# Kernel tuning notes

Measured on AMD Instinct MI355X. Metric: run time of the kernel, lower is better.

The kernel has to match this reference:

```python
import jax, jax.numpy as jnp
import numpy as np
from jax import lax

N, H, C_IN, G, E_CLS, N_ACT = 8192, 128, 3, 40, 16, 5
FLAT = 8 * 8 * 32  # conv output 8x8x32 for grid_size=40


def _conv(x, w, b, stride):
    y = lax.conv_general_dilated(x, w, (stride, stride), 'VALID',
                                 dimension_numbers=('NCHW', 'OIHW', 'NCHW'))
    return y + b[None, :, None, None]


def setup_inputs() -> dict:
    key = jax.random.key(0)
    ks = jax.random.split(key, 24)
    s = 0.05
    return {
        'img_batch': jax.random.normal(ks[0], (N, C_IN, G, G), jnp.float32),
        'adjacency': jax.random.randint(ks[1], (N, N), 0, 2, jnp.int32),
        'class_ids': jax.random.randint(ks[2], (N,), 0, 2, jnp.int64),
        'hidden_state': jax.random.normal(ks[3], (N, H), jnp.float32),
        'conv1_w': jax.random.normal(ks[4], (16, C_IN, 5, 5), jnp.float32) * s,
        'conv1_b': jnp.zeros((16,), jnp.float32),
        'conv2_w': jax.random.normal(ks[5], (32, 16, 3, 3), jnp.float32) * s,
        'conv2_b': jnp.zeros((32,), jnp.float32),
        'fc_vis_w': jax.random.normal(ks[6], (H, FLAT), jnp.float32) * s,
        'fc_vis_b': jnp.zeros((H,), jnp.float32),
        'embed_table': jax.random.normal(ks[7], (2, E_CLS), jnp.float32) * s,
        'gru_w_ih': jax.random.normal(ks[8], (3 * H, H + E_CLS), jnp.float32) * s,
        'gru_w_hh': jax.random.normal(ks[9], (3 * H, H), jnp.float32) * s,
        'gru_b_ih': jnp.zeros((3 * H,), jnp.float32),
        'gru_b_hh': jnp.zeros((3 * H,), jnp.float32),
        'wq_w': jax.random.normal(ks[10], (H, H), jnp.float32) * s,
        'wq_b': jnp.zeros((H,), jnp.float32),
        'wk_w': jax.random.normal(ks[11], (H, H), jnp.float32) * s,
        'wk_b': jnp.zeros((H,), jnp.float32),
        'wv_w': jax.random.normal(ks[12], (H, H), jnp.float32) * s,
        'wv_b': jnp.zeros((H,), jnp.float32),
        'attn_out_w': jax.random.normal(ks[13], (H, H), jnp.float32) * s,
        'attn_out_b': jnp.zeros((H,), jnp.float32),
        'fcq_w': jax.random.normal(ks[14], (N_ACT, 2 * H), jnp.float32) * s,
        'fcq_b': jnp.zeros((N_ACT,), jnp.float32),
    }


def reference(img_batch, adjacency, class_ids, hidden_state,
              conv1_w, conv1_b, conv2_w, conv2_b,
              fc_vis_w, fc_vis_b, embed_table,
              gru_w_ih, gru_w_hh, gru_b_ih, gru_b_hh,
              wq_w, wq_b, wk_w, wk_b, wv_w, wv_b,
              attn_out_w, attn_out_b, fcq_w, fcq_b):
    # CNN encoder
    x = jax.nn.relu(_conv(img_batch, conv1_w, conv1_b, 2))
    x = jax.nn.relu(_conv(x, conv2_w, conv2_b, 2))
    x = x.reshape(x.shape[0], -1)  # [N, 2048]
    vis_feat = jax.nn.relu(x @ fc_vis_w.T + fc_vis_b)
    cls_feat = embed_table[class_ids]  # [N, 16]
    feat = jnp.concatenate([vis_feat, cls_feat], axis=1)  # [N, 144]
    # GRUCell (torch semantics)
    gi = feat @ gru_w_ih.T + gru_b_ih
    gh = hidden_state @ gru_w_hh.T + gru_b_hh
    i_r, i_z, i_n = jnp.split(gi, 3, axis=1)
    h_r, h_z, h_n = jnp.split(gh, 3, axis=1)
    r = jax.nn.sigmoid(i_r + h_r)
    z = jax.nn.sigmoid(i_z + h_z)
    n = jnp.tanh(i_n + r * h_n)
    new_hidden = (1.0 - z) * n + z * hidden_state
    # Swarm attention with adjacency mask (dropout = identity in eval)
    Q = new_hidden @ wq_w.T + wq_b
    K = new_hidden @ wk_w.T + wk_b
    V = new_hidden @ wv_w.T + wv_b
    scores = (Q @ K.T) / jnp.sqrt(jnp.float32(H))  # [N, N]
    scores = jnp.where(adjacency == 0, jnp.float32(-1e9), scores)
    attn = jax.nn.softmax(scores, axis=-1)
    context = attn @ V
    swarm_context = context @ attn_out_w.T + attn_out_b
    combined = jnp.concatenate([new_hidden, swarm_context], axis=1)
    q_values = combined @ fcq_w.T + fcq_b
    return q_values, new_hidden
```

## Files before the change

### kernel.cpp

```cpp
#include <hip/hip_runtime.h>

typedef __bf16 bf16x8 __attribute__((ext_vector_type(8)));
typedef float f32x4 __attribute__((ext_vector_type(4)));

#define L2E 1.4426950408889634f

__global__ __launch_bounds__(256, 2) void conv_fused(
    const float* __restrict__ img, const float* __restrict__ w1, const float* __restrict__ b1,
    const float* __restrict__ w2, const float* __restrict__ b2, float* __restrict__ flat) {
  __shared__ float simg[4800];
  __shared__ float sc1[5184];
  __shared__ float sw1[1200];
  __shared__ float sw2[32 * 145];
  __shared__ float sb1[16];
  __shared__ float sb2[32];
  const int n = blockIdx.x;
  const int t = threadIdx.x;
  const float* ib = img + (size_t)n * 4800;
  for (int i = t; i < 4800; i += 256) simg[i] = ib[i];
  for (int i = t; i < 1200; i += 256) sw1[i] = w1[i];
  for (int i = t; i < 4608; i += 256) {
    const int oc = i / 144, rem = i - oc * 144;
    sw2[oc * 145 + rem] = w2[i];
  }
  if (t < 16) sb1[t] = b1[t];
  else if (t < 48) sb2[t - 16] = b2[t - 16];
  __syncthreads();

  {
    const int oc = t & 15;
    float wr[75];
#pragma unroll
    for (int i = 0; i < 75; ++i) wr[i] = sw1[oc * 75 + i];
    const float bias = sb1[oc];
#pragma unroll 1
    for (int q = (t >> 4); q < 81; q += 16) {
      const int qy = q / 9, qx = q - qy * 9;
      float a00 = bias, a01 = bias, a10 = bias, a11 = bias;
#pragma unroll
      for (int ic = 0; ic < 3; ++ic) {
        float rg[7][7];
        const int base = ic * 1600 + qy * 160 + qx * 4;
#pragma unroll
        for (int row = 0; row < 7; ++row) {
          const float* rp = &simg[base + row * 40];
          const float2 v0 = *(const float2*)(rp);
          const float2 v1 = *(const float2*)(rp + 2);
          const float2 v2 = *(const float2*)(rp + 4);
          rg[row][0] = v0.x; rg[row][1] = v0.y; rg[row][2] = v1.x; rg[row][3] = v1.y;
          rg[row][4] = v2.x; rg[row][5] = v2.y; rg[row][6] = rp[6];
        }
#pragma unroll
        for (int ky = 0; ky < 5; ++ky)
#pragma unroll
          for (int kx = 0; kx < 5; ++kx) {
            const float wv = wr[ic * 25 + ky * 5 + kx];
            a00 = fmaf(rg[ky][kx], wv, a00);
            a01 = fmaf(rg[ky][kx + 2], wv, a01);
            a10 = fmaf(rg[ky + 2][kx], wv, a10);
            a11 = fmaf(rg[ky + 2][kx + 2], wv, a11);
          }
      }
      const int o = oc * 324 + qy * 36 + qx * 2;
      sc1[o] = fmaxf(a00, 0.f);
      sc1[o + 1] = fmaxf(a01, 0.f);
      sc1[o + 18] = fmaxf(a10, 0.f);
      sc1[o + 19] = fmaxf(a11, 0.f);
    }
  }
  __syncthreads();

  float* sc2 = simg;
  {
    const int oc = t & 31;
    float wr[144];
#pragma unroll
    for (int i = 0; i < 144; ++i) wr[i] = sw2[oc * 145 + i];
    const float bias = sb2[oc];
#pragma unroll 1
    for (int q = (t >> 5); q < 16; q += 8) {
      const int qy = q >> 2, qx = q & 3;
      float a00 = bias, a01 = bias, a10 = bias, a11 = bias;
#pragma unroll
      for (int ic = 0; ic < 16; ++ic) {
        float rg[5][5];
        const int base = ic * 324 + qy * 72 + qx * 4;
#pragma unroll
        for (int row = 0; row < 5; ++row) {
          const float* rp = &sc1[base + row * 18];
          const float2 v0 = *(const float2*)(rp);
          const float2 v1 = *(const float2*)(rp + 2);
          rg[row][0] = v0.x; rg[row][1] = v0.y; rg[row][2] = v1.x; rg[row][3] = v1.y;
          rg[row][4] = rp[4];
        }
#pragma unroll
        for (int ky = 0; ky < 3; ++ky)
#pragma unroll
          for (int kx = 0; kx < 3; ++kx) {
            const float wv = wr[ic * 9 + ky * 3 + kx];
            a00 = fmaf(rg[ky][kx], wv, a00);
            a01 = fmaf(rg[ky][kx + 2], wv, a01);
            a10 = fmaf(rg[ky + 2][kx], wv, a10);
            a11 = fmaf(rg[ky + 2][kx + 2], wv, a11);
          }
      }
      const int o = oc * 64 + qy * 16 + qx * 2;
      sc2[o] = fmaxf(a00, 0.f);
      sc2[o + 1] = fmaxf(a01, 0.f);
      sc2[o + 8] = fmaxf(a10, 0.f);
      sc2[o + 9] = fmaxf(a11, 0.f);
    }
  }
  __syncthreads();
  float* ob = flat + (size_t)n * 2048;
  for (int i = t; i < 2048; i += 256) ob[i] = sc2[i];
}

template <int EPI>
__global__ __launch_bounds__(256) void gemm_nt(
    const float* __restrict__ A, const float* __restrict__ W, const float* __restrict__ bias,
    float* __restrict__ C, int M, int N, int K, int lda, int ldw, int ldc) {
  __shared__ float As[32][36];
  __shared__ float Ws[32][132];
  const int t = threadIdx.x;
  const int m0 = blockIdx.x * 32, n0 = blockIdx.y * 128;
  const int ty = t >> 6, tx = t & 63;
  float acc[8][2];
#pragma unroll
  for (int i = 0; i < 8; ++i) { acc[i][0] = 0.f; acc[i][1] = 0.f; }
  const int arow = t >> 3, akc = (t & 7) * 4;
  const int wrow = t >> 1, wkh = (t & 1) * 16;
  for (int k0 = 0; k0 < K; k0 += 32) {
    float4 av = {0.f, 0.f, 0.f, 0.f};
    if (k0 + akc < K)
      av = *reinterpret_cast<const float4*>(&A[(size_t)(m0 + arow) * lda + k0 + akc]);
    float4 wv[4];
#pragma unroll
    for (int j = 0; j < 4; ++j) {
      wv[j] = {0.f, 0.f, 0.f, 0.f};
      if (k0 + wkh + 4 * j < K)
        wv[j] = *reinterpret_cast<const float4*>(&W[(size_t)(n0 + wrow) * ldw + k0 + wkh + 4 * j]);
    }
    __syncthreads();
    As[akc + 0][arow] = av.x; As[akc + 1][arow] = av.y;
    As[akc + 2][arow] = av.z; As[akc + 3][arow] = av.w;
#pragma unroll
    for (int j = 0; j < 4; ++j) {
      Ws[wkh + 4 * j + 0][wrow] = wv[j].x; Ws[wkh + 4 * j + 1][wrow] = wv[j].y;
      Ws[wkh + 4 * j + 2][wrow] = wv[j].z; Ws[wkh + 4 * j + 3][wrow] = wv[j].w;
    }
    __syncthreads();
#pragma unroll
    for (int kk = 0; kk < 32; ++kk) {
      const float4 a0 = *reinterpret_cast<const float4*>(&As[kk][ty * 8]);
      const float4 a1 = *reinterpret_cast<const float4*>(&As[kk][ty * 8 + 4]);
      const float2 b = *reinterpret_cast<const float2*>(&Ws[kk][tx * 2]);
      float ar[8];
      ar[0] = a0.x; ar[1] = a0.y; ar[2] = a0.z; ar[3] = a0.w;
      ar[4] = a1.x; ar[5] = a1.y; ar[6] = a1.z; ar[7] = a1.w;
#pragma unroll
      for (int i = 0; i < 8; ++i) {
        acc[i][0] = fmaf(ar[i], b.x, acc[i][0]);
        acc[i][1] = fmaf(ar[i], b.y, acc[i][1]);
      }
    }
  }
  const float b0 = bias[n0 + tx * 2], b1 = bias[n0 + tx * 2 + 1];
#pragma unroll
  for (int i = 0; i < 8; ++i) {
    float r0 = acc[i][0] + b0, r1 = acc[i][1] + b1;
    if (EPI == 1) { r0 = fmaxf(r0, 0.f); r1 = fmaxf(r1, 0.f); }
    float2 o; o.x = r0; o.y = r1;
    *reinterpret_cast<float2*>(&C[(size_t)(m0 + ty * 8 + i) * ldc + n0 + tx * 2]) = o;
  }
}

__global__ void embed_fill(const int* __restrict__ cid, const float* __restrict__ emb,
                           float* __restrict__ feat) {
  const int id = blockIdx.x * 256 + threadIdx.x;
  const int n = id >> 4, e = id & 15;
  feat[n * 144 + 128 + e] = emb[cid[n] * 16 + e];
}

__global__ void gru_gates(const float* __restrict__ gi, const float* __restrict__ gh,
                          const float* __restrict__ h, float* __restrict__ nh) {
  const int id = blockIdx.x * 256 + threadIdx.x;
  const int n = id >> 7, j = id & 127;
  const int b = n * 384 + j;
  const float r = 1.f / (1.f + __expf(-(gi[b] + gh[b])));
  const float z = 1.f / (1.f + __expf(-(gi[b + 128] + gh[b + 128])));
  const float nn = tanhf(gi[b + 256] + r * gh[b + 256]);
  nh[id] = (1.f - z) * nn + z * h[id];
}

__global__ __launch_bounds__(256) void pack_qkv(
    const float* __restrict__ Qf, const float* __restrict__ Kf, const float* __restrict__ Vf,
    __bf16* __restrict__ Qb, __bf16* __restrict__ Kb, __bf16* __restrict__ Vt) {
  __shared__ float sv[64][132];
  const int t = threadIdx.x;
  const int m0 = blockIdx.x * 64;
  for (int i = t; i < 8192; i += 256) {
    const int mm = i >> 7, c = i & 127;
    const int g = (m0 + mm) * 128 + c;
    Qb[g] = (__bf16)(Qf[g] * 0.08838834764831845f);
    Kb[g] = (__bf16)Kf[g];
    sv[mm][c] = Vf[g];
  }
  __syncthreads();
  const int d = t >> 1, mh = (t & 1) * 32;
#pragma unroll
  for (int g8 = 0; g8 < 4; ++g8) {
    bf16x8 v;
#pragma unroll
    for (int j = 0; j < 8; ++j) v[j] = (__bf16)sv[mh + g8 * 8 + j][d];
    *reinterpret_cast<bf16x8*>(&Vt[(size_t)d * 8192 + m0 + mh + g8 * 8]) = v;
  }
}

__global__ __launch_bounds__(256, 2) void flash_attn(
    const __bf16* __restrict__ Qb, const __bf16* __restrict__ Kb, const __bf16* __restrict__ Vt,
    const int* __restrict__ adj, float* __restrict__ Opart,
    float* __restrict__ Marr, float* __restrict__ Larr) {
  __shared__ __bf16 Klds[64 * 128];
  __shared__ __bf16 Vlds[128 * 64];
  __shared__ __bf16 Plds[4][16 * 72];
  const int t = threadIdx.x;
  const int w = t >> 6, l = t & 63;
  const int lr = l & 15, lg = l >> 4;
  const int qbase = blockIdx.x * 64 + w * 16;
  const int split = blockIdx.y;

  bf16x8 qf[4];
#pragma unroll
  for (int kk = 0; kk < 4; ++kk)
    qf[kk] = *reinterpret_cast<const bf16x8*>(&Qb[(qbase + lr) * 128 + kk * 32 + lg * 8]);

  f32x4 accO[8];
#pragma unroll
  for (int n = 0; n < 8; ++n) accO[n] = f32x4{0.f, 0.f, 0.f, 0.f};
  float mrow[4] = {-1e9f, -1e9f, -1e9f, -1e9f};
  float lrow[4] = {0.f, 0.f, 0.f, 0.f};

  const int j0 = split * 2048, j1 = j0 + 2048;
  for (int jt = j0; jt < j1; jt += 64) {
#pragma unroll
    for (int i = 0; i < 4; ++i) {
      const int idx = i * 256 + t;
      {
        const int row = idx >> 4, c = idx & 15;
        const uint4 v = *reinterpret_cast<const uint4*>(&Kb[(size_t)(jt + row) * 128 + c * 8]);
        *reinterpret_cast<uint4*>(&Klds[row * 128 + ((c ^ (row & 7)) * 8)]) = v;
      }
      {
        const int d = idx >> 3, c = idx & 7;
        const uint4 v = *reinterpret_cast<const uint4*>(&Vt[(size_t)d * 8192 + jt + c * 8]);
        *reinterpret_cast<uint4*>(&Vlds[d * 64 + ((c ^ (d & 7)) * 8)]) = v;
      }
    }
    __syncthreads();

    f32x4 sacc[4];
#pragma unroll
    for (int st = 0; st < 4; ++st) {
      f32x4 a = f32x4{0.f, 0.f, 0.f, 0.f};
      const int jl = st * 16 + lr;
#pragma unroll
      for (int kk = 0; kk < 4; ++kk) {
        const bf16x8 kf = *reinterpret_cast<const bf16x8*>(
            &Klds[jl * 128 + (((kk * 4 + lg) ^ (jl & 7)) * 8)]);
        a = __builtin_amdgcn_mfma_f32_16x16x32_bf16(qf[kk], kf, a, 0, 0, 0);
      }
      sacc[st] = a;
    }

    float smv[4][4];
#pragma unroll
    for (int st = 0; st < 4; ++st) {
      const int jj = jt + st * 16 + lr;
#pragma unroll
      for (int r = 0; r < 4; ++r) {
        const int av = adj[(size_t)(qbase + lg * 4 + r) * 8192 + jj];
        smv[st][r] = (av != 0) ? sacc[st][r] : -1e9f;
      }
    }
    float p[4][4], alpha[4];
#pragma unroll
    for (int r = 0; r < 4; ++r) {
      float tm = fmaxf(fmaxf(smv[0][r], smv[1][r]), fmaxf(smv[2][r], smv[3][r]));
      tm = fmaxf(tm, __shfl_xor(tm, 1));
      tm = fmaxf(tm, __shfl_xor(tm, 2));
      tm = fmaxf(tm, __shfl_xor(tm, 4));
      tm = fmaxf(tm, __shfl_xor(tm, 8));
      const float mnew = fmaxf(mrow[r], tm);
      alpha[r] = exp2f((mrow[r] - mnew) * L2E);
      mrow[r] = mnew;
      float ps = 0.f;
#pragma unroll
      for (int st = 0; st < 4; ++st) {
        const float pv = exp2f((smv[st][r] - mnew) * L2E);
        p[st][r] = pv;
        ps += pv;
      }
      lrow[r] = lrow[r] * alpha[r] + ps;
    }
#pragma unroll
    for (int n = 0; n < 8; ++n) {
#pragma unroll
      for (int r = 0; r < 4; ++r) accO[n][r] *= alpha[r];
    }

    __bf16* pw = &Plds[w][0];
#pragma unroll
    for (int st = 0; st < 4; ++st)
#pragma unroll
      for (int r = 0; r < 4; ++r)
        pw[(lg * 4 + r) * 72 + st * 16 + lr] = (__bf16)p[st][r];
    bf16x8 pf[2];
#pragma unroll
    for (int ks = 0; ks < 2; ++ks)
      pf[ks] = *reinterpret_cast<const bf16x8*>(&pw[lr * 72 + ks * 32 + lg * 8]);

#pragma unroll
    for (int n = 0; n < 8; ++n) {
      const int dl = n * 16 + lr;
#pragma unroll
      for (int ks = 0; ks < 2; ++ks) {
        const bf16x8 vf = *reinterpret_cast<const bf16x8*>(
            &Vlds[dl * 64 + (((ks * 4 + lg) ^ (dl & 7)) * 8)]);
        accO[n] = __builtin_amdgcn_mfma_f32_16x16x32_bf16(pf[ks], vf, accO[n], 0, 0, 0);
      }
    }
    __syncthreads();
  }

#pragma unroll
  for (int r = 0; r < 4; ++r) {
    float ls = lrow[r];
    ls += __shfl_xor(ls, 1); ls += __shfl_xor(ls, 2);
    ls += __shfl_xor(ls, 4); ls += __shfl_xor(ls, 8);
    if (lr == 0) {
      const int qrow = qbase + lg * 4 + r;
      Marr[split * 8192 + qrow] = mrow[r];
      Larr[split * 8192 + qrow] = ls;
    }
  }
#pragma unroll
  for (int n = 0; n < 8; ++n)
#pragma unroll
    for (int r = 0; r < 4; ++r) {
      const int qrow = qbase + lg * 4 + r;
      Opart[(size_t)(split * 8192 + qrow) * 128 + n * 16 + lr] = accO[n][r];
    }
}

__global__ void combine_kernel(const float* __restrict__ Opart, const float* __restrict__ Marr,
                               const float* __restrict__ Larr, float* __restrict__ ctx) {
  const int id = blockIdx.x * 256 + threadIdx.x;
  const int m = id >> 5, d4 = (id & 31) * 4;
  const float m0 = Marr[m], m1 = Marr[8192 + m], m2 = Marr[16384 + m], m3 = Marr[24576 + m];
  const float ms = fmaxf(fmaxf(m0, m1), fmaxf(m2, m3));
  const float w0 = exp2f((m0 - ms) * L2E), w1 = exp2f((m1 - ms) * L2E);
  const float w2 = exp2f((m2 - ms) * L2E), w3 = exp2f((m3 - ms) * L2E);
  const float den = w0 * Larr[m] + w1 * Larr[8192 + m] + w2 * Larr[16384 + m] + w3 * Larr[24576 + m];
  const float4 o0 = *reinterpret_cast<const float4*>(&Opart[(size_t)m * 128 + d4]);
  const float4 o1 = *reinterpret_cast<const float4*>(&Opart[(size_t)(8192 + m) * 128 + d4]);
  const float4 o2 = *reinterpret_cast<const float4*>(&Opart[(size_t)(16384 + m) * 128 + d4]);
  const float4 o3 = *reinterpret_cast<const float4*>(&Opart[(size_t)(24576 + m) * 128 + d4]);
  const float inv = 1.f / den;
  float4 r;
  r.x = (w0 * o0.x + w1 * o1.x + w2 * o2.x + w3 * o3.x) * inv;
  r.y = (w0 * o0.y + w1 * o1.y + w2 * o2.y + w3 * o3.y) * inv;
  r.z = (w0 * o0.z + w1 * o1.z + w2 * o2.z + w3 * o3.z) * inv;
  r.w = (w0 * o0.w + w1 * o1.w + w2 * o2.w + w3 * o3.w) * inv;
  *reinterpret_cast<float4*>(&ctx[(size_t)m * 128 + d4]) = r;
}

__global__ void fcq_kernel(const float* __restrict__ newh, const float* __restrict__ swarm,
                           const float* __restrict__ fw, const float* __restrict__ fb,
                           float* __restrict__ qout) {
  const int id = blockIdx.x * 256 + threadIdx.x;
  const int row = id / 5, a = id - row * 5;
  const float4* x0 = reinterpret_cast<const float4*>(newh + (size_t)row * 128);
  const float4* x1 = reinterpret_cast<const float4*>(swarm + (size_t)row * 128);
  const float4* wv = reinterpret_cast<const float4*>(fw + a * 256);
  float acc = fb[a];
#pragma unroll
  for (int i = 0; i < 32; ++i) {
    const float4 x = x0[i], ww = wv[i];
    acc += x.x * ww.x + x.y * ww.y + x.z * ww.z + x.w * ww.w;
  }
#pragma unroll
  for (int i = 0; i < 32; ++i) {
    const float4 x = x1[i], ww = wv[32 + i];
    acc += x.x * ww.x + x.y * ww.y + x.z * ww.z + x.w * ww.w;
  }
  qout[id] = acc;
}

extern "C" void kernel_launch(void* const* d_in, const int* in_sizes, int n_in,
                              void* d_out, int out_size, void* d_ws, size_t ws_size,
                              hipStream_t stream) {
  const float* img    = (const float*)d_in[0];
  const int*   adj    = (const int*)d_in[1];
  const int*   cid    = (const int*)d_in[2];
  const float* hidden = (const float*)d_in[3];
  const float* w1  = (const float*)d_in[4];  const float* b1  = (const float*)d_in[5];
  const float* w2  = (const float*)d_in[6];  const float* b2  = (const float*)d_in[7];
  const float* fcw = (const float*)d_in[8];  const float* fcb = (const float*)d_in[9];
  const float* emb = (const float*)d_in[10];
  const float* wih = (const float*)d_in[11]; const float* whh = (const float*)d_in[12];
  const float* bih = (const float*)d_in[13]; const float* bhh = (const float*)d_in[14];
  const float* wq  = (const float*)d_in[15]; const float* wqb = (const float*)d_in[16];
  const float* wk  = (const float*)d_in[17]; const float* wkb = (const float*)d_in[18];
  const float* wv  = (const float*)d_in[19]; const float* wvb = (const float*)d_in[20];
  const float* wo  = (const float*)d_in[21]; const float* wob = (const float*)d_in[22];
  const float* fqw = (const float*)d_in[23]; const float* fqb = (const float*)d_in[24];

  float* out  = (float*)d_out;
  float* qout = out;
  float* newh = out + 8192 * 5;

  char* ws = (char*)d_ws;
  float* flat  = (float*)(ws + 0);
  float* gi    = (float*)(ws + 0);
  float* gh    = (float*)(ws + 12582912);
  float* Qf    = (float*)(ws + 25165824);
  float* Kf    = (float*)(ws + 29360128);
  float* Vf    = (float*)(ws + 33554432);
  __bf16* Qb   = (__bf16*)(ws + 37748736);
  __bf16* Kb   = (__bf16*)(ws + 39845888);
  __bf16* Vt   = (__bf16*)(ws + 41943040);
  float* Opart = (float*)(ws + 44040192);
  float* Marr  = (float*)(ws + 60817408);
  float* Larr  = (float*)(ws + 60948480);
  float* ctx   = (float*)(ws + 61079552);
  float* swarm = (float*)(ws + 0);
  float* feat  = (float*)(ws + 67108864);

  conv_fused<<<8192, 256, 0, stream>>>(img, w1, b1, w2, b2, flat);
  gemm_nt<1><<<dim3(256, 1), 256, 0, stream>>>(flat, fcw, fcb, feat, 8192, 128, 2048, 2048, 2048, 144);
  embed_fill<<<512, 256, 0, stream>>>(cid, emb, feat);
  gemm_nt<0><<<dim3(256, 3), 256, 0, stream>>>(feat, wih, bih, gi, 8192, 384, 144, 144, 144, 384);
  gemm_nt<0><<<dim3(256, 3), 256, 0, stream>>>(hidden, whh, bhh, gh, 8192, 384, 128, 128, 128, 384);
  gru_gates<<<4096, 256, 0, stream>>>(gi, gh, hidden, newh);
  gemm_nt<0><<<dim3(256, 1), 256, 0, stream>>>(newh, wq, wqb, Qf, 8192, 128, 128, 128, 128, 128);
  gemm_nt<0><<<dim3(256, 1), 256, 0, stream>>>(newh, wk, wkb, Kf, 8192, 128, 128, 128, 128, 128);
  gemm_nt<0><<<dim3(256, 1), 256, 0, stream>>>(newh, wv, wvb, Vf, 8192, 128, 128, 128, 128, 128);
  pack_qkv<<<128, 256, 0, stream>>>(Qf, Kf, Vf, Qb, Kb, Vt);
  flash_attn<<<dim3(128, 4), 256, 0, stream>>>(Qb, Kb, Vt, adj, Opart, Marr, Larr);
  combine_kernel<<<1024, 256, 0, stream>>>(Opart, Marr, Larr, ctx);
  gemm_nt<0><<<dim3(256, 1), 256, 0, stream>>>(ctx, wo, wob, swarm, 8192, 128, 128, 128, 128, 128);
  fcq_kernel<<<160, 256, 0, stream>>>(newh, swarm, fqw, fqb, qout);
}
```

Measured before the change: 1.115 ms.

## Restructure conv kernel, double-buffer smaller-tile GEMM, raise occupancy bounds

The fused conv kernel no longer stages weights in shared memory. Each thread now handles two output channels and streams weights from global memory per input channel, which cuts register and LDS pressure so four blocks can be resident per CU. The generic GEMM switches to 32x64 tiles with double-buffered LDS, launching twice as many blocks and overlapping global loads with compute. The flash attention launch bound rises to 3 blocks per CU and one score array is reused in place. Together these aim to raise occupancy and latency hiding, at the cost of more global weight loads in conv and possible register spills.

```diff
diff --git a/kernel.cpp b/kernel.cpp
--- a/kernel.cpp
+++ b/kernel.cpp
@@ -5,111 +5,139 @@
 
 #define L2E 1.4426950408889634f
 
-__global__ __launch_bounds__(256, 2) void conv_fused(
+__global__ __launch_bounds__(256, 4) void conv_fused(
     const float* __restrict__ img, const float* __restrict__ w1, const float* __restrict__ b1,
     const float* __restrict__ w2, const float* __restrict__ b2, float* __restrict__ flat) {
   __shared__ float simg[4800];
   __shared__ float sc1[5184];
-  __shared__ float sw1[1200];
-  __shared__ float sw2[32 * 145];
-  __shared__ float sb1[16];
-  __shared__ float sb2[32];
-  const int n = blockIdx.x;
-  const int t = threadIdx.x;
+  const int n = blockIdx.x, t = threadIdx.x;
   const float* ib = img + (size_t)n * 4800;
   for (int i = t; i < 4800; i += 256) simg[i] = ib[i];
-  for (int i = t; i < 1200; i += 256) sw1[i] = w1[i];
-  for (int i = t; i < 4608; i += 256) {
-    const int oc = i / 144, rem = i - oc * 144;
-    sw2[oc * 145 + rem] = w2[i];
-  }
-  if (t < 16) sb1[t] = b1[t];
-  else if (t < 48) sb2[t - 16] = b2[t - 16];
   __syncthreads();
 
   {
-    const int oc = t & 15;
-    float wr[75];
-#pragma unroll
-    for (int i = 0; i < 75; ++i) wr[i] = sw1[oc * 75 + i];
-    const float bias = sb1[oc];
-#pragma unroll 1
-    for (int q = (t >> 4); q < 81; q += 16) {
-      const int qy = q / 9, qx = q - qy * 9;
-      float a00 = bias, a01 = bias, a10 = bias, a11 = bias;
-#pragma unroll
-      for (int ic = 0; ic < 3; ++ic) {
-        float rg[7][7];
-        const int base = ic * 1600 + qy * 160 + qx * 4;
-#pragma unroll
-        for (int row = 0; row < 7; ++row) {
-          const float* rp = &simg[base + row * 40];
-          const float2 v0 = *(const float2*)(rp);
-          const float2 v1 = *(const float2*)(rp + 2);
-          const float2 v2 = *(const float2*)(rp + 4);
-          rg[row][0] = v0.x; rg[row][1] = v0.y; rg[row][2] = v1.x; rg[row][3] = v1.y;
-          rg[row][4] = v2.x; rg[row][5] = v2.y; rg[row][6] = rp[6];
+    const int oc = t & 7, qslot = t >> 3;
+    float acc[3][2][4];
+    const float bA = b1[oc], bB = b1[oc + 8];
+#pragma unroll
+    for (int qi = 0; qi < 3; ++qi)
+#pragma unroll
+      for (int j = 0; j < 4; ++j) { acc[qi][0][j] = bA; acc[qi][1][j] = bB; }
+#pragma unroll
+    for (int ic = 0; ic < 3; ++ic) {
+      float wA[25], wB[25];
+      const float* wpA = w1 + oc * 75 + ic * 25;
+      const float* wpB = w1 + (oc + 8) * 75 + ic * 25;
+#pragma unroll
+      for (int i = 0; i < 25; ++i) { wA[i] = wpA[i]; wB[i] = wpB[i]; }
+#pragma unroll
+      for (int qi = 0; qi < 3; ++qi) {
+        const int q = qslot + qi * 32;
+        if (q < 81) {
+          const int qy = q / 9, qx = q - qy * 9;
+          const int base = ic * 1600 + qy * 160 + qx * 4;
+#pragma unroll
+          for (int row = 0; row < 7; ++row) {
+            const float* rp = &simg[base + row * 40];
+            const float4 v0 = *(const float4*)rp;
+            const float2 v1 = *(const float2*)(rp + 4);
+            float rr[7];
+            rr[0] = v0.x; rr[1] = v0.y; rr[2] = v0.z; rr[3] = v0.w;
+            rr[4] = v1.x; rr[5] = v1.y; rr[6] = rp[6];
+            if (row < 5) {
+#pragma unroll
+              for (int kx = 0; kx < 5; ++kx) {
+                const float wa = wA[row * 5 + kx], wb = wB[row * 5 + kx];
+                acc[qi][0][0] = fmaf(rr[kx], wa, acc[qi][0][0]);
+                acc[qi][0][1] = fmaf(rr[kx + 2], wa, acc[qi][0][1]);
+                acc[qi][1][0] = fmaf(rr[kx], wb, acc[qi][1][0]);
+                acc[qi][1][1] = fmaf(rr[kx + 2], wb, acc[qi][1][1]);
+              }
+            }
+            if (row >= 2) {
+#pragma unroll
+              for (int kx = 0; kx < 5; ++kx) {
+                const float wa = wA[(row - 2) * 5 + kx], wb = wB[(row - 2) * 5 + kx];
+                acc[qi][0][2] = fmaf(rr[kx], wa, acc[qi][0][2]);
+                acc[qi][0][3] = fmaf(rr[kx + 2], wa, acc[qi][0][3]);
+                acc[qi][1][2] = fmaf(rr[kx], wb, acc[qi][1][2]);
+                acc[qi][1][3] = fmaf(rr[kx + 2], wb, acc[qi][1][3]);
+              }
+            }
+          }
         }
-#pragma unroll
-        for (int ky = 0; ky < 5; ++ky)
-#pragma unroll
-          for (int kx = 0; kx < 5; ++kx) {
-            const float wv = wr[ic * 25 + ky * 5 + kx];
-            a00 = fmaf(rg[ky][kx], wv, a00);
-            a01 = fmaf(rg[ky][kx + 2], wv, a01);
-            a10 = fmaf(rg[ky + 2][kx], wv, a10);
-            a11 = fmaf(rg[ky + 2][kx + 2], wv, a11);
-          }
-      }
-      const int o = oc * 324 + qy * 36 + qx * 2;
-      sc1[o] = fmaxf(a00, 0.f);
-      sc1[o + 1] = fmaxf(a01, 0.f);
-      sc1[o + 18] = fmaxf(a10, 0.f);
-      sc1[o + 19] = fmaxf(a11, 0.f);
+      }
+    }
+#pragma unroll
+    for (int qi = 0; qi < 3; ++qi) {
+      const int q = qslot + qi * 32;
+      if (q < 81) {
+        const int qy = q / 9, qx = q - qy * 9;
+#pragma unroll
+        for (int p = 0; p < 2; ++p) {
+          const int o = (oc + p * 8) * 324 + qy * 36 + qx * 2;
+          float2 top, bot;
+          top.x = fmaxf(acc[qi][p][0], 0.f); top.y = fmaxf(acc[qi][p][1], 0.f);
+          bot.x = fmaxf(acc[qi][p][2], 0.f); bot.y = fmaxf(acc[qi][p][3], 0.f);
+          *(float2*)&sc1[o] = top;
+          *(float2*)&sc1[o + 18] = bot;
+        }
+      }
     }
   }
   __syncthreads();
 
   float* sc2 = simg;
   {
-    const int oc = t & 31;
-    float wr[144];
-#pragma unroll
-    for (int i = 0; i < 144; ++i) wr[i] = sw2[oc * 145 + i];
-    const float bias = sb2[oc];
-#pragma unroll 1
-    for (int q = (t >> 5); q < 16; q += 8) {
-      const int qy = q >> 2, qx = q & 3;
-      float a00 = bias, a01 = bias, a10 = bias, a11 = bias;
-#pragma unroll
-      for (int ic = 0; ic < 16; ++ic) {
-        float rg[5][5];
-        const int base = ic * 324 + qy * 72 + qx * 4;
-#pragma unroll
-        for (int row = 0; row < 5; ++row) {
-          const float* rp = &sc1[base + row * 18];
-          const float2 v0 = *(const float2*)(rp);
-          const float2 v1 = *(const float2*)(rp + 2);
-          rg[row][0] = v0.x; rg[row][1] = v0.y; rg[row][2] = v1.x; rg[row][3] = v1.y;
-          rg[row][4] = rp[4];
+    const int oc = t & 15, qslot = t >> 4;
+    const int qy = qslot >> 2, qx = qslot & 3;
+    float accA[4], accB[4];
+    const float bA = b2[oc], bB = b2[oc + 16];
+#pragma unroll
+    for (int j = 0; j < 4; ++j) { accA[j] = bA; accB[j] = bB; }
+#pragma unroll
+    for (int ic = 0; ic < 16; ++ic) {
+      float wA[9], wB[9];
+      const float* wpA = w2 + oc * 144 + ic * 9;
+      const float* wpB = w2 + (oc + 16) * 144 + ic * 9;
+#pragma unroll
+      for (int i = 0; i < 9; ++i) { wA[i] = wpA[i]; wB[i] = wpB[i]; }
+      const int base = ic * 324 + qy * 72 + qx * 4;
+#pragma unroll
+      for (int row = 0; row < 5; ++row) {
+        const float* rp = &sc1[base + row * 18];
+        const float2 v0 = *(const float2*)rp;
+        const float2 v1 = *(const float2*)(rp + 2);
+        float rr[5];
+        rr[0] = v0.x; rr[1] = v0.y; rr[2] = v1.x; rr[3] = v1.y; rr[4] = rp[4];
+        if (row < 3) {
+#pragma unroll
+          for (int kx = 0; kx < 3; ++kx) {
+            const float wa = wA[row * 3 + kx], wb = wB[row * 3 + kx];
+            accA[0] = fmaf(rr[kx], wa, accA[0]);
+            accA[1] = fmaf(rr[kx + 2], wa, accA[1]);
+            accB[0] = fmaf(rr[kx], wb, accB[0]);
+            accB[1] = fmaf(rr[kx + 2], wb, accB[1]);
+          }
         }
-#pragma unroll
-        for (int ky = 0; ky < 3; ++ky)
+        if (row >= 2) {
 #pragma unroll
           for (int kx = 0; kx < 3; ++kx) {
-            const float wv = wr[ic * 9 + ky * 3 + kx];
-            a00 = fmaf(rg[ky][kx], wv, a00);
-            a01 = fmaf(rg[ky][kx + 2], wv, a01);
-            a10 = fmaf(rg[ky + 2][kx], wv, a10);
-            a11 = fmaf(rg[ky + 2][kx + 2], wv, a11);
+            const float wa = wA[(row - 2) * 3 + kx], wb = wB[(row - 2) * 3 + kx];
+            accA[2] = fmaf(rr[kx], wa, accA[2]);
+            accA[3] = fmaf(rr[kx + 2], wa, accA[3]);
+            accB[2] = fmaf(rr[kx], wb, accB[2]);
+            accB[3] = fmaf(rr[kx + 2], wb, accB[3]);
           }
-      }
-      const int o = oc * 64 + qy * 16 + qx * 2;
-      sc2[o] = fmaxf(a00, 0.f);
-      sc2[o + 1] = fmaxf(a01, 0.f);
-      sc2[o + 8] = fmaxf(a10, 0.f);
-      sc2[o + 9] = fmaxf(a11, 0.f);
-    }
+        }
+      }
+    }
+    const int oA = oc * 64 + qy * 16 + qx * 2;
+    const int oB = (oc + 16) * 64 + qy * 16 + qx * 2;
+    sc2[oA] = fmaxf(accA[0], 0.f); sc2[oA + 1] = fmaxf(accA[1], 0.f);
+    sc2[oA + 8] = fmaxf(accA[2], 0.f); sc2[oA + 9] = fmaxf(accA[3], 0.f);
+    sc2[oB] = fmaxf(accB[0], 0.f); sc2[oB + 1] = fmaxf(accB[1], 0.f);
+    sc2[oB + 8] = fmaxf(accB[2], 0.f); sc2[oB + 9] = fmaxf(accB[3], 0.f);
   }
   __syncthreads();
   float* ob = flat + (size_t)n * 2048;
@@ -120,58 +148,65 @@
 __global__ __launch_bounds__(256) void gemm_nt(
     const float* __restrict__ A, const float* __restrict__ W, const float* __restrict__ bias,
     float* __restrict__ C, int M, int N, int K, int lda, int ldw, int ldc) {
-  __shared__ float As[32][36];
-  __shared__ float Ws[32][132];
+  __shared__ float As[2][32][36];
+  __shared__ float Ws[2][32][66];
   const int t = threadIdx.x;
-  const int m0 = blockIdx.x * 32, n0 = blockIdx.y * 128;
-  const int ty = t >> 6, tx = t & 63;
-  float acc[8][2];
-#pragma unroll
-  for (int i = 0; i < 8; ++i) { acc[i][0] = 0.f; acc[i][1] = 0.f; }
-  const int arow = t >> 3, akc = (t & 7) * 4;
-  const int wrow = t >> 1, wkh = (t & 1) * 16;
-  for (int k0 = 0; k0 < K; k0 += 32) {
-    float4 av = {0.f, 0.f, 0.f, 0.f};
-    if (k0 + akc < K)
-      av = *reinterpret_cast<const float4*>(&A[(size_t)(m0 + arow) * lda + k0 + akc]);
-    float4 wv[4];
-#pragma unroll
-    for (int j = 0; j < 4; ++j) {
-      wv[j] = {0.f, 0.f, 0.f, 0.f};
-      if (k0 + wkh + 4 * j < K)
-        wv[j] = *reinterpret_cast<const float4*>(&W[(size_t)(n0 + wrow) * ldw + k0 + wkh + 4 * j]);
-    }
+  const int m0 = blockIdx.x * 32, n0 = blockIdx.y * 64;
+  const int arow = t >> 3, ak = (t & 7) * 4;
+  const int wrow = t >> 2, wk = (t & 3) * 8;
+  const int tm = t >> 5, tn = t & 31;
+  float acc[4][2] = {{0.f, 0.f}, {0.f, 0.f}, {0.f, 0.f}, {0.f, 0.f}};
+  float4 av, wv0, wv1;
+
+  auto load_g = [&](int k0) {
+    av = float4{0.f, 0.f, 0.f, 0.f};
+    wv0 = float4{0.f, 0.f, 0.f, 0.f};
+    wv1 = float4{0.f, 0.f, 0.f, 0.f};
+    if (k0 + ak < K) av = *(const float4*)&A[(size_t)(m0 + arow) * lda + k0 + ak];
+    if (k0 + wk < K) wv0 = *(const float4*)&W[(size_t)(n0 + wrow) * ldw + k0 + wk];
+    if (k0 + wk + 4 < K) wv1 = *(const float4*)&W[(size_t)(n0 + wrow) * ldw + k0 + wk + 4];
+  };
+  auto store_l = [&](int buf) {
+    As[buf][ak + 0][arow] = av.x; As[buf][ak + 1][arow] = av.y;
+    As[buf][ak + 2][arow] = av.z; As[buf][ak + 3][arow] = av.w;
+    Ws[buf][wk + 0][wrow] = wv0.x; Ws[buf][wk + 1][wrow] = wv0.y;
+    Ws[buf][wk + 2][wrow] = wv0.z; Ws[buf][wk + 3][wrow] = wv0.w;
+    Ws[buf][wk + 4][wrow] = wv1.x; Ws[buf][wk + 5][wrow] = wv1.y;
+    Ws[buf][wk + 6][wrow] = wv1.z; Ws[buf][wk + 7][wrow] = wv1.w;
+  };
+  auto compute = [&](int buf) {
+#pragma unroll
+    for (int kk = 0; kk < 32; ++kk) {
+      const float4 a = *(const float4*)&As[buf][kk][tm * 4];
+      const float2 b = *(const float2*)&Ws[buf][kk][tn * 2];
+      acc[0][0] = fmaf(a.x, b.x, acc[0][0]); acc[0][1] = fmaf(a.x, b.y, acc[0][1]);
+      acc[1][0] = fmaf(a.y, b.x, acc[1][0]); acc[1][1] = fmaf(a.y, b.y, acc[1][1]);
+      acc[2][0] = fmaf(a.z, b.x, acc[2][0]); acc[2][1] = fmaf(a.z, b.y, acc[2][1]);
+      acc[3][0] = fmaf(a.w, b.x, acc[3][0]); acc[3][1] = fmaf(a.w, b.y, acc[3][1]);
+    }
+  };
+
+  load_g(0);
+  store_l(0);
+  __syncthreads();
+  int cur = 0;
+  for (int k0 = 32; k0 < K; k0 += 32) {
+    load_g(k0);
+    compute(cur);
     __syncthreads();
-    As[akc + 0][arow] = av.x; As[akc + 1][arow] = av.y;
-    As[akc + 2][arow] = av.z; As[akc + 3][arow] = av.w;
-#pragma unroll
-    for (int j = 0; j < 4; ++j) {
-      Ws[wkh + 4 * j + 0][wrow] = wv[j].x; Ws[wkh + 4 * j + 1][wrow] = wv[j].y;
-      Ws[wkh + 4 * j + 2][wrow] = wv[j].z; Ws[wkh + 4 * j + 3][wrow] = wv[j].w;
-    }
+    store_l(cur ^ 1);
     __syncthreads();
-#pragma unroll
-    for (int kk = 0; kk < 32; ++kk) {
-      const float4 a0 = *reinterpret_cast<const float4*>(&As[kk][ty * 8]);
-      const float4 a1 = *reinterpret_cast<const float4*>(&As[kk][ty * 8 + 4]);
-      const float2 b = *reinterpret_cast<const float2*>(&Ws[kk][tx * 2]);
-      float ar[8];
-      ar[0] = a0.x; ar[1] = a0.y; ar[2] = a0.z; ar[3] = a0.w;
-      ar[4] = a1.x; ar[5] = a1.y; ar[6] = a1.z; ar[7] = a1.w;
-#pragma unroll
-      for (int i = 0; i < 8; ++i) {
-        acc[i][0] = fmaf(ar[i], b.x, acc[i][0]);
-        acc[i][1] = fmaf(ar[i], b.y, acc[i][1]);
-      }
-    }
-  }
-  const float b0 = bias[n0 + tx * 2], b1 = bias[n0 + tx * 2 + 1];
-#pragma unroll
-  for (int i = 0; i < 8; ++i) {
+    cur ^= 1;
+  }
+  compute(cur);
+
+  const float b0 = bias[n0 + tn * 2], b1 = bias[n0 + tn * 2 + 1];
+#pragma unroll
+  for (int i = 0; i < 4; ++i) {
     float r0 = acc[i][0] + b0, r1 = acc[i][1] + b1;
     if (EPI == 1) { r0 = fmaxf(r0, 0.f); r1 = fmaxf(r1, 0.f); }
     float2 o; o.x = r0; o.y = r1;
-    *reinterpret_cast<float2*>(&C[(size_t)(m0 + ty * 8 + i) * ldc + n0 + tx * 2]) = o;
+    *(float2*)&C[(size_t)(m0 + tm * 4 + i) * ldc + n0 + tn * 2] = o;
   }
 }
 
@@ -217,7 +252,7 @@
   }
 }
 
-__global__ __launch_bounds__(256, 2) void flash_attn(
+__global__ __launch_bounds__(256, 3) void flash_attn(
     const __bf16* __restrict__ Qb, const __bf16* __restrict__ Kb, const __bf16* __restrict__ Vt,
     const int* __restrict__ adj, float* __restrict__ Opart,
     float* __restrict__ Marr, float* __restrict__ Larr) {
@@ -273,20 +308,20 @@
       sacc[st] = a;
     }
 
-    float smv[4][4];
+    float pv[4][4];
 #pragma unroll
     for (int st = 0; st < 4; ++st) {
       const int jj = jt + st * 16 + lr;
 #pragma unroll
       for (int r = 0; r < 4; ++r) {
         const int av = adj[(size_t)(qbase + lg * 4 + r) * 8192 + jj];
-        smv[st][r] = (av != 0) ? sacc[st][r] : -1e9f;
-      }
-    }
-    float p[4][4], alpha[4];
+        pv[st][r] = (av != 0) ? sacc[st][r] : -1e9f;
+      }
+    }
+    float alpha[4];
 #pragma unroll
     for (int r = 0; r < 4; ++r) {
-      float tm = fmaxf(fmaxf(smv[0][r], smv[1][r]), fmaxf(smv[2][r], smv[3][r]));
+      float tm = fmaxf(fmaxf(pv[0][r], pv[1][r]), fmaxf(pv[2][r], pv[3][r]));
       tm = fmaxf(tm, __shfl_xor(tm, 1));
       tm = fmaxf(tm, __shfl_xor(tm, 2));
       tm = fmaxf(tm, __shfl_xor(tm, 4));
@@ -297,9 +332,9 @@
       float ps = 0.f;
 #pragma unroll
       for (int st = 0; st < 4; ++st) {
-        const float pv = exp2f((smv[st][r] - mnew) * L2E);
-        p[st][r] = pv;
-        ps += pv;
+        const float e = exp2f((pv[st][r] - mnew) * L2E);
+        pv[st][r] = e;
+        ps += e;
       }
       lrow[r] = lrow[r] * alpha[r] + ps;
     }
@@ -314,7 +349,7 @@
     for (int st = 0; st < 4; ++st)
 #pragma unroll
       for (int r = 0; r < 4; ++r)
-        pw[(lg * 4 + r) * 72 + st * 16 + lr] = (__bf16)p[st][r];
+        pw[(lg * 4 + r) * 72 + st * 16 + lr] = (__bf16)pv[st][r];
     bf16x8 pf[2];
 #pragma unroll
     for (int ks = 0; ks < 2; ++ks)
@@ -438,17 +473,17 @@
   float* feat  = (float*)(ws + 67108864);
 
   conv_fused<<<8192, 256, 0, stream>>>(img, w1, b1, w2, b2, flat);
-  gemm_nt<1><<<dim3(256, 1), 256, 0, stream>>>(flat, fcw, fcb, feat, 8192, 128, 2048, 2048, 2048, 144);
+  gemm_nt<1><<<dim3(256, 2), 256, 0, stream>>>(flat, fcw, fcb, feat, 8192, 128, 2048, 2048, 2048, 144);
   embed_fill<<<512, 256, 0, stream>>>(cid, emb, feat);
-  gemm_nt<0><<<dim3(256, 3), 256, 0, stream>>>(feat, wih, bih, gi, 8192, 384, 144, 144, 144, 384);
-  gemm_nt<0><<<dim3(256, 3), 256, 0, stream>>>(hidden, whh, bhh, gh, 8192, 384, 128, 128, 128, 384);
+  gemm_nt<0><<<dim3(256, 6), 256, 0, stream>>>(feat, wih, bih, gi, 8192, 384, 144, 144, 144, 384);
+  gemm_nt<0><<<dim3(256, 6), 256, 0, stream>>>(hidden, whh, bhh, gh, 8192, 384, 128, 128, 128, 384);
   gru_gates<<<4096, 256, 0, stream>>>(gi, gh, hidden, newh);
-  gemm_nt<0><<<dim3(256, 1), 256, 0, stream>>>(newh, wq, wqb, Qf, 8192, 128, 128, 128, 128, 128);
-  gemm_nt<0><<<dim3(256, 1), 256, 0, stream>>>(newh, wk, wkb, Kf, 8192, 128, 128, 128, 128, 128);
-  gemm_nt<0><<<dim3(256, 1), 256, 0, stream>>>(newh, wv, wvb, Vf, 8192, 128, 128, 128, 128, 128);
+  gemm_nt<0><<<dim3(256, 2), 256, 0, stream>>>(newh, wq, wqb, Qf, 8192, 128, 128, 128, 128, 128);
+  gemm_nt<0><<<dim3(256, 2), 256, 0, stream>>>(newh, wk, wkb, Kf, 8192, 128, 128, 128, 128, 128);
+  gemm_nt<0><<<dim3(256, 2), 256, 0, stream>>>(newh, wv, wvb, Vf, 8192, 128, 128, 128, 128, 128);
   pack_qkv<<<128, 256, 0, stream>>>(Qf, Kf, Vf, Qb, Kb, Vt);
   flash_attn<<<dim3(128, 4), 256, 0, stream>>>(Qb, Kb, Vt, adj, Opart, Marr, Larr);
   combine_kernel<<<1024, 256, 0, stream>>>(Opart, Marr, Larr, ctx);
-  gemm_nt<0><<<dim3(256, 1), 256, 0, stream>>>(ctx, wo, wob, swarm, 8192, 128, 128, 128, 128, 128);
+  gemm_nt<0><<<dim3(256, 2), 256, 0, stream>>>(ctx, wo, wob, swarm, 8192, 128, 128, 128, 128, 128);
   fcq_kernel<<<160, 256, 0, stream>>>(newh, swarm, fqw, fqb, qout);
 }
```

After: 1.042 ms. -6.6%, faster.
